# Performance work log

Hardware: AMD Instinct MI355X
Metric: run time of the kernel (lower is better)

The kernel has to match this reference:

```python
import jax, jax.numpy as jnp
import numpy as np

N_NODES = 50000
N_EDGES = 800000
D_NODE = 64
D_EDGE = 64
D_GLOBAL = 16
D_IN = D_EDGE + 2 * D_NODE + D_GLOBAL  # 208
D_HID = 256
D_OUT = 64


def setup_inputs() -> dict:
    key = jax.random.key(0)
    ks = jax.random.split(key, 8)
    x = jax.random.normal(ks[0], (N_NODES, D_NODE), dtype=jnp.float32)
    edge_attr = jax.random.normal(ks[1], (N_EDGES, D_EDGE), dtype=jnp.float32)
    u = jax.random.normal(ks[2], (1, D_GLOBAL), dtype=jnp.float32)
    W1 = jax.random.normal(ks[3], (D_IN, D_HID), dtype=jnp.float32) * (1.0 / np.sqrt(D_IN))
    b1 = jnp.zeros((D_HID,), dtype=jnp.float32)
    W2 = jax.random.normal(ks[4], (D_HID, D_OUT), dtype=jnp.float32) * (1.0 / np.sqrt(D_HID))
    b2 = jnp.zeros((D_OUT,), dtype=jnp.float32)
    edge_index = jax.random.randint(ks[5], (2, N_EDGES), 0, N_NODES, dtype=jnp.int64)
    return {"x": x, "edge_attr": edge_attr, "u": u, "W1": W1, "b1": b1,
            "W2": W2, "b2": b2, "edge_index": edge_index}


def reference(x, edge_attr, u, W1, b1, W2, b2, edge_index):
    E = edge_attr.shape[0]
    recv = x[edge_index[1]]                         # [E, D_NODE] receiver gather
    send = x[edge_index[0]]                         # [E, D_NODE] sender gather
    g = jnp.broadcast_to(u, (E, u.shape[-1]))       # [E, D_GLOBAL] globals broadcast
    collected = jnp.concatenate([edge_attr, recv, send, g], axis=-1)  # [E, 208]
    h = jax.nn.relu(collected @ W1 + b1)            # [E, 256]
    updated_edges = h @ W2 + b2                     # [E, 64]
    return updated_edges
```

## Files before the change

### kernel.cpp

```cpp
#include <hip/hip_runtime.h>
#include <hip/hip_bf16.h>


#define N_EDGES   800000
#define N_TILES   (N_EDGES / 16)
#define K1        192
#define D_HID     256
#define D_OUT     64
#define W1T_LD    200
#define W2T_LD    264
#define WAVES_PB  16
#define BLOCK_T   (WAVES_PB * 64)
#define GRID_MAIN 256

typedef __attribute__((ext_vector_type(8))) short  short8;
typedef __attribute__((ext_vector_type(4))) float  floatx4;

#define WS_W1T_OFF 0
#define WS_W2T_OFF (256 * W1T_LD * 2)
#define WS_B1P_OFF (WS_W2T_OFF + 64 * W2T_LD * 2)

static __device__ __forceinline__ unsigned short f2bf(float f) {
    unsigned u = __builtin_bit_cast(unsigned, f);
    u += 0x7fffu + ((u >> 16) & 1u);
    return (unsigned short)(u >> 16);
}

static __device__ __forceinline__ short8 cvt8(const float* __restrict__ p) {
    const floatx4* p4 = (const floatx4*)p;
    floatx4 f0 = p4[0];
    floatx4 f1 = p4[1];
    union { short8 s8; unsigned short us[8]; } u;
    u.us[0] = f2bf(f0.x); u.us[1] = f2bf(f0.y); u.us[2] = f2bf(f0.z); u.us[3] = f2bf(f0.w);
    u.us[4] = f2bf(f1.x); u.us[5] = f2bf(f1.y); u.us[6] = f2bf(f1.z); u.us[7] = f2bf(f1.w);
    return u.s8;
}

__global__ void edgeblk_prep(const float* __restrict__ W1, const float* __restrict__ b1,
                             const float* __restrict__ W2, const float* __restrict__ u,
                             unsigned short* __restrict__ w1t, unsigned short* __restrict__ w2t,
                             float* __restrict__ b1p) {
    int tid = blockIdx.x * blockDim.x + threadIdx.x;
    int nth = gridDim.x * blockDim.x;
    for (int j = tid; j < 256 * K1; j += nth) {
        int n = j / K1, k = j - n * K1;
        w1t[n * W1T_LD + k] = f2bf(W1[k * 256 + n]);
    }
    for (int j = tid; j < 64 * 256; j += nth) {
        int m = j >> 8, k = j & 255;
        int kap = k & 31, q = kap >> 3, t = kap & 7;
        int rho = (t < 4) ? (q * 4 + t) : (16 + q * 4 + (t - 4));
        int src = (k & ~31) + rho;
        w2t[m * W2T_LD + k] = f2bf(W2[src * 64 + m]);
    }
    for (int n = tid; n < 256; n += nth) {
        float s = b1[n];
        for (int t = 0; t < 16; ++t) s += u[t] * W1[(K1 + t) * 256 + n];
        b1p[n] = s;
    }
}

__global__ __launch_bounds__(BLOCK_T) void edgeblk_mlp(
        const float* __restrict__ x, const float* __restrict__ edge_attr,
        const int* __restrict__ eidx,
        const unsigned short* __restrict__ w1t_g, const unsigned short* __restrict__ w2t_g,
        const float* __restrict__ b1p_g, const float* __restrict__ b2_g,
        float* __restrict__ out) {
    __shared__ alignas(16) unsigned short sW1[256 * W1T_LD];
    __shared__ alignas(16) unsigned short sW2[64 * W2T_LD];
    __shared__ alignas(16) float sB1[256];
    __shared__ alignas(16) float sB2[64];

    {
        const uint4* s1 = (const uint4*)w1t_g;  uint4* d1 = (uint4*)sW1;
        for (int i = threadIdx.x; i < 256 * W1T_LD / 8; i += BLOCK_T) d1[i] = s1[i];
        const uint4* s2 = (const uint4*)w2t_g;  uint4* d2 = (uint4*)sW2;
        for (int i = threadIdx.x; i < 64 * W2T_LD / 8; i += BLOCK_T) d2[i] = s2[i];
        if (threadIdx.x < 256) sB1[threadIdx.x] = b1p_g[threadIdx.x];
        if (threadIdx.x < 64)  sB2[threadIdx.x] = b2_g[threadIdx.x];
    }
    __syncthreads();

    const int wid  = threadIdx.x >> 6;
    const int lane = threadIdx.x & 63;
    const int m    = lane & 15;
    const int quad = lane >> 4;

    float b2v[4];
#pragma unroll
    for (int nt = 0; nt < 4; ++nt) b2v[nt] = sB2[nt * 16 + m];

    const int gw = blockIdx.x * WAVES_PB + wid;
    const int NW = GRID_MAIN * WAVES_PB;

    for (int tile = gw; tile < N_TILES; tile += NW) {
        const int e    = tile * 16 + m;
        const int recv = eidx[N_EDGES + e];
        const int send = eidx[e];
        const float* pe = edge_attr + (long)e    * 64 + quad * 8;
        const float* pr = x         + (long)recv * 64 + quad * 8;
        const float* ps = x         + (long)send * 64 + quad * 8;

        short8 A[6];
        A[0] = cvt8(pe);      A[1] = cvt8(pe + 32);
        A[2] = cvt8(pr);      A[3] = cvt8(pr + 32);
        A[4] = cvt8(ps);      A[5] = cvt8(ps + 32);

        floatx4 oacc[4];
#pragma unroll
        for (int nt = 0; nt < 4; ++nt) oacc[nt] = (floatx4){0.f, 0.f, 0.f, 0.f};

#pragma unroll
        for (int nc = 0; nc < 8; ++nc) {
            floatx4 c0 = (floatx4){0.f, 0.f, 0.f, 0.f};
            floatx4 c1 = (floatx4){0.f, 0.f, 0.f, 0.f};
#pragma unroll
            for (int kt = 0; kt < 6; ++kt) {
                short8 bA = *(const short8*)&sW1[(nc * 32      + m) * W1T_LD + kt * 32 + quad * 8];
                short8 bB = *(const short8*)&sW1[(nc * 32 + 16 + m) * W1T_LD + kt * 32 + quad * 8];
                c0 = __builtin_amdgcn_mfma_f32_16x16x32_bf16(bA, A[kt], c0, 0, 0, 0);
                c1 = __builtin_amdgcn_mfma_f32_16x16x32_bf16(bB, A[kt], c1, 0, 0, 0);
            }
            const floatx4 bias0 = *(const floatx4*)&sB1[nc * 32      + quad * 4];
            const floatx4 bias1 = *(const floatx4*)&sB1[nc * 32 + 16 + quad * 4];
            union { short8 s8; unsigned short us[8]; } a2u;
#pragma unroll
            for (int r = 0; r < 4; ++r) {
                float h0 = c0[r] + bias0[r];
                float h1 = c1[r] + bias1[r];
                h0 = h0 > 0.f ? h0 : 0.f;
                h1 = h1 > 0.f ? h1 : 0.f;
                a2u.us[r]     = f2bf(h0);
                a2u.us[r + 4] = f2bf(h1);
            }
            short8 a2 = a2u.s8;
#pragma unroll
            for (int nt = 0; nt < 4; ++nt) {
                short8 b2f = *(const short8*)&sW2[(nt * 16 + m) * W2T_LD + nc * 32 + quad * 8];
                oacc[nt] = __builtin_amdgcn_mfma_f32_16x16x32_bf16(a2, b2f, oacc[nt], 0, 0, 0);
            }
        }

        float* po = out + (long)tile * 16 * 64;
#pragma unroll
        for (int nt = 0; nt < 4; ++nt) {
#pragma unroll
            for (int r = 0; r < 4; ++r) {
                po[(quad * 4 + r) * 64 + nt * 16 + m] = oacc[nt][r] + b2v[nt];
            }
        }
    }
}

extern "C" void kernel_launch(void* const* d_in, const int* in_sizes, int n_in,
                              void* d_out, int out_size, void* d_ws, size_t ws_size,
                              hipStream_t stream) {
    const float* x   = (const float*)d_in[0];
    const float* ea  = (const float*)d_in[1];
    const float* u   = (const float*)d_in[2];
    const float* W1  = (const float*)d_in[3];
    const float* b1  = (const float*)d_in[4];
    const float* W2  = (const float*)d_in[5];
    const float* b2  = (const float*)d_in[6];
    const int*   ei  = (const int*)d_in[7];
    float* out = (float*)d_out;

    unsigned short* w1t = (unsigned short*)((char*)d_ws + WS_W1T_OFF);
    unsigned short* w2t = (unsigned short*)((char*)d_ws + WS_W2T_OFF);
    float*          b1p = (float*)((char*)d_ws + WS_B1P_OFF);

    hipLaunchKernelGGL(edgeblk_prep, dim3(192), dim3(256), 0, stream,
                       W1, b1, W2, u, w1t, w2t, b1p);
    hipLaunchKernelGGL(edgeblk_mlp, dim3(GRID_MAIN), dim3(BLOCK_T), 0, stream,
                       x, ea, ei, w1t, w2t, b1p, b2, out);
}
```

Before: 2.022 ms.

## Pre-convert node features to bf16, prefetch gathers, transpose output MFMA for vector stores

```diff
diff --git a/kernel.cpp b/kernel.cpp
--- a/kernel.cpp
+++ b/kernel.cpp
@@ -2,6 +2,7 @@
 #include <hip/hip_bf16.h>
 
 
+#define N_NODES   50000
 #define N_EDGES   800000
 #define N_TILES   (N_EDGES / 16)
 #define K1        192
@@ -19,6 +20,7 @@
 #define WS_W1T_OFF 0
 #define WS_W2T_OFF (256 * W1T_LD * 2)
 #define WS_B1P_OFF (WS_W2T_OFF + 64 * W2T_LD * 2)
+#define WS_XB_OFF  (WS_B1P_OFF + 1024)
 
 static __device__ __forceinline__ unsigned short f2bf(float f) {
     unsigned u = __builtin_bit_cast(unsigned, f);
@@ -26,20 +28,25 @@
     return (unsigned short)(u >> 16);
 }
 
-static __device__ __forceinline__ short8 cvt8(const float* __restrict__ p) {
-    const floatx4* p4 = (const floatx4*)p;
-    floatx4 f0 = p4[0];
-    floatx4 f1 = p4[1];
+static __device__ __forceinline__ short8 pack8(floatx4 f0, floatx4 f1) {
     union { short8 s8; unsigned short us[8]; } u;
     u.us[0] = f2bf(f0.x); u.us[1] = f2bf(f0.y); u.us[2] = f2bf(f0.z); u.us[3] = f2bf(f0.w);
     u.us[4] = f2bf(f1.x); u.us[5] = f2bf(f1.y); u.us[6] = f2bf(f1.z); u.us[7] = f2bf(f1.w);
     return u.s8;
 }
 
+static __device__ __forceinline__ short8 cvt8nt(const float* __restrict__ p) {
+    const floatx4* p4 = (const floatx4*)p;
+    floatx4 f0 = __builtin_nontemporal_load(p4);
+    floatx4 f1 = __builtin_nontemporal_load(p4 + 1);
+    return pack8(f0, f1);
+}
+
 __global__ void edgeblk_prep(const float* __restrict__ W1, const float* __restrict__ b1,
                              const float* __restrict__ W2, const float* __restrict__ u,
+                             const float* __restrict__ x,
                              unsigned short* __restrict__ w1t, unsigned short* __restrict__ w2t,
-                             float* __restrict__ b1p) {
+                             float* __restrict__ b1p, unsigned short* __restrict__ xb) {
     int tid = blockIdx.x * blockDim.x + threadIdx.x;
     int nth = gridDim.x * blockDim.x;
     for (int j = tid; j < 256 * K1; j += nth) {
@@ -58,10 +65,15 @@
         for (int t = 0; t < 16; ++t) s += u[t] * W1[(K1 + t) * 256 + n];
         b1p[n] = s;
     }
-}
-
-__global__ __launch_bounds__(BLOCK_T) void edgeblk_mlp(
-        const float* __restrict__ x, const float* __restrict__ edge_attr,
+    short8* xb8 = (short8*)xb;
+    for (int j = tid; j < N_NODES * 64 / 8; j += nth) {
+        const floatx4* p4 = (const floatx4*)(x + j * 8);
+        xb8[j] = pack8(p4[0], p4[1]);
+    }
+}
+
+__global__ __launch_bounds__(BLOCK_T, 4) void edgeblk_mlp(
+        const unsigned short* __restrict__ xb, const float* __restrict__ edge_attr,
         const int* __restrict__ eidx,
         const unsigned short* __restrict__ w1t_g, const unsigned short* __restrict__ w2t_g,
         const float* __restrict__ b1p_g, const float* __restrict__ b2_g,
@@ -86,25 +98,49 @@
     const int m    = lane & 15;
     const int quad = lane >> 4;
 
-    float b2v[4];
-#pragma unroll
-    for (int nt = 0; nt < 4; ++nt) b2v[nt] = sB2[nt * 16 + m];
-
     const int gw = blockIdx.x * WAVES_PB + wid;
     const int NW = GRID_MAIN * WAVES_PB;
 
-    for (int tile = gw; tile < N_TILES; tile += NW) {
-        const int e    = tile * 16 + m;
-        const int recv = eidx[N_EDGES + e];
-        const int send = eidx[e];
-        const float* pe = edge_attr + (long)e    * 64 + quad * 8;
-        const float* pr = x         + (long)recv * 64 + quad * 8;
-        const float* ps = x         + (long)send * 64 + quad * 8;
-
+    int tile = gw;
+    short8 Rp0 = {}, Rp1 = {}, Sp0 = {}, Sp1 = {};
+    int rcv1 = 0, snd1 = 0;
+    if (tile < N_TILES) {
+        int e = tile * 16 + m;
+        int rcv = eidx[N_EDGES + e];
+        int snd = eidx[e];
+        const short8* pr = (const short8*)(xb + (long)rcv * 64 + quad * 8);
+        Rp0 = pr[0]; Rp1 = pr[4];
+        const short8* ps = (const short8*)(xb + (long)snd * 64 + quad * 8);
+        Sp0 = ps[0]; Sp1 = ps[4];
+    }
+    if (tile + NW < N_TILES) {
+        int e = (tile + NW) * 16 + m;
+        rcv1 = eidx[N_EDGES + e];
+        snd1 = eidx[e];
+    }
+
+    for (; tile < N_TILES; tile += NW) {
         short8 A[6];
-        A[0] = cvt8(pe);      A[1] = cvt8(pe + 32);
-        A[2] = cvt8(pr);      A[3] = cvt8(pr + 32);
-        A[4] = cvt8(ps);      A[5] = cvt8(ps + 32);
+        A[2] = Rp0; A[3] = Rp1; A[4] = Sp0; A[5] = Sp1;
+        const float* pe = edge_attr + (long)(tile * 16 + m) * 64 + quad * 8;
+        A[0] = cvt8nt(pe);
+        A[1] = cvt8nt(pe + 32);
+
+        {
+            int tn = tile + NW;
+            if (tn < N_TILES) {
+                const short8* pr = (const short8*)(xb + (long)rcv1 * 64 + quad * 8);
+                Rp0 = pr[0]; Rp1 = pr[4];
+                const short8* ps = (const short8*)(xb + (long)snd1 * 64 + quad * 8);
+                Sp0 = ps[0]; Sp1 = ps[4];
+                int t2 = tn + NW;
+                if (t2 < N_TILES) {
+                    int e2 = t2 * 16 + m;
+                    rcv1 = eidx[N_EDGES + e2];
+                    snd1 = eidx[e2];
+                }
+            }
+        }
 
         floatx4 oacc[4];
 #pragma unroll
@@ -137,17 +173,18 @@
 #pragma unroll
             for (int nt = 0; nt < 4; ++nt) {
                 short8 b2f = *(const short8*)&sW2[(nt * 16 + m) * W2T_LD + nc * 32 + quad * 8];
-                oacc[nt] = __builtin_amdgcn_mfma_f32_16x16x32_bf16(a2, b2f, oacc[nt], 0, 0, 0);
+                oacc[nt] = __builtin_amdgcn_mfma_f32_16x16x32_bf16(b2f, a2, oacc[nt], 0, 0, 0);
             }
         }
 
-        float* po = out + (long)tile * 16 * 64;
+        float* po = out + (long)tile * 16 * 64 + m * 64;
 #pragma unroll
         for (int nt = 0; nt < 4; ++nt) {
-#pragma unroll
-            for (int r = 0; r < 4; ++r) {
-                po[(quad * 4 + r) * 64 + nt * 16 + m] = oacc[nt][r] + b2v[nt];
-            }
+            const floatx4 bb = *(const floatx4*)&sB2[nt * 16 + quad * 4];
+            floatx4 v;
+#pragma unroll
+            for (int r = 0; r < 4; ++r) v[r] = oacc[nt][r] + bb[r];
+            __builtin_nontemporal_store(v, (floatx4*)(po + nt * 16 + quad * 4));
         }
     }
 }
@@ -168,9 +205,10 @@
     unsigned short* w1t = (unsigned short*)((char*)d_ws + WS_W1T_OFF);
     unsigned short* w2t = (unsigned short*)((char*)d_ws + WS_W2T_OFF);
     float*          b1p = (float*)((char*)d_ws + WS_B1P_OFF);
-
-    hipLaunchKernelGGL(edgeblk_prep, dim3(192), dim3(256), 0, stream,
-                       W1, b1, W2, u, w1t, w2t, b1p);
+    unsigned short* xb  = (unsigned short*)((char*)d_ws + WS_XB_OFF);
+
+    hipLaunchKernelGGL(edgeblk_prep, dim3(256), dim3(256), 0, stream,
+                       W1, b1, W2, u, x, w1t, w2t, b1p, xb);
     hipLaunchKernelGGL(edgeblk_mlp, dim3(GRID_MAIN), dim3(BLOCK_T), 0, stream,
-                       x, ea, ei, w1t, w2t, b1p, b2, out);
-}
+                       xb, ea, ei, w1t, w2t, b1p, b2, out);
+}
```

Result: slower. 2.137 ms (+5.7%).

## Pre-convert node features to bf16 and vectorize output stores via swapped MFMA operands

Applied to the files above, without the earlier changes.

```diff
diff --git a/kernel.cpp b/kernel.cpp
--- a/kernel.cpp
+++ b/kernel.cpp
@@ -2,6 +2,7 @@
 #include <hip/hip_bf16.h>
 
 
+#define N_NODES   50000
 #define N_EDGES   800000
 #define N_TILES   (N_EDGES / 16)
 #define K1        192
@@ -19,6 +20,7 @@
 #define WS_W1T_OFF 0
 #define WS_W2T_OFF (256 * W1T_LD * 2)
 #define WS_B1P_OFF (WS_W2T_OFF + 64 * W2T_LD * 2)
+#define WS_XB_OFF  (WS_B1P_OFF + 1024)
 
 static __device__ __forceinline__ unsigned short f2bf(float f) {
     unsigned u = __builtin_bit_cast(unsigned, f);
@@ -26,20 +28,23 @@
     return (unsigned short)(u >> 16);
 }
 
-static __device__ __forceinline__ short8 cvt8(const float* __restrict__ p) {
-    const floatx4* p4 = (const floatx4*)p;
-    floatx4 f0 = p4[0];
-    floatx4 f1 = p4[1];
+static __device__ __forceinline__ short8 pack8(floatx4 f0, floatx4 f1) {
     union { short8 s8; unsigned short us[8]; } u;
     u.us[0] = f2bf(f0.x); u.us[1] = f2bf(f0.y); u.us[2] = f2bf(f0.z); u.us[3] = f2bf(f0.w);
     u.us[4] = f2bf(f1.x); u.us[5] = f2bf(f1.y); u.us[6] = f2bf(f1.z); u.us[7] = f2bf(f1.w);
     return u.s8;
 }
 
+static __device__ __forceinline__ short8 cvt8(const float* __restrict__ p) {
+    const floatx4* p4 = (const floatx4*)p;
+    return pack8(p4[0], p4[1]);
+}
+
 __global__ void edgeblk_prep(const float* __restrict__ W1, const float* __restrict__ b1,
                              const float* __restrict__ W2, const float* __restrict__ u,
+                             const float* __restrict__ x,
                              unsigned short* __restrict__ w1t, unsigned short* __restrict__ w2t,
-                             float* __restrict__ b1p) {
+                             float* __restrict__ b1p, unsigned short* __restrict__ xb) {
     int tid = blockIdx.x * blockDim.x + threadIdx.x;
     int nth = gridDim.x * blockDim.x;
     for (int j = tid; j < 256 * K1; j += nth) {
@@ -58,10 +63,17 @@
         for (int t = 0; t < 16; ++t) s += u[t] * W1[(K1 + t) * 256 + n];
         b1p[n] = s;
     }
+    short8* xb8 = (short8*)xb;
+    for (int j = tid; j < N_NODES * 64 / 8; j += nth) {
+        const floatx4* p4 = (const floatx4*)(x + j * 8);
+        xb8[j] = pack8(p4[0], p4[1]);
+    }
 }
 
-__global__ __launch_bounds__(BLOCK_T) void edgeblk_mlp(
-        const float* __restrict__ x, const float* __restrict__ edge_attr,
+__global__ __launch_bounds__(BLOCK_T)
+__attribute__((amdgpu_waves_per_eu(4, 4)))
+void edgeblk_mlp(
+        const unsigned short* __restrict__ xb, const float* __restrict__ edge_attr,
         const int* __restrict__ eidx,
         const unsigned short* __restrict__ w1t_g, const unsigned short* __restrict__ w2t_g,
         const float* __restrict__ b1p_g, const float* __restrict__ b2_g,
@@ -86,10 +98,6 @@
     const int m    = lane & 15;
     const int quad = lane >> 4;
 
-    float b2v[4];
-#pragma unroll
-    for (int nt = 0; nt < 4; ++nt) b2v[nt] = sB2[nt * 16 + m];
-
     const int gw = blockIdx.x * WAVES_PB + wid;
     const int NW = GRID_MAIN * WAVES_PB;
 
@@ -97,14 +105,17 @@
         const int e    = tile * 16 + m;
         const int recv = eidx[N_EDGES + e];
         const int send = eidx[e];
-        const float* pe = edge_attr + (long)e    * 64 + quad * 8;
-        const float* pr = x         + (long)recv * 64 + quad * 8;
-        const float* ps = x         + (long)send * 64 + quad * 8;
 
         short8 A[6];
-        A[0] = cvt8(pe);      A[1] = cvt8(pe + 32);
-        A[2] = cvt8(pr);      A[3] = cvt8(pr + 32);
-        A[4] = cvt8(ps);      A[5] = cvt8(ps + 32);
+        {
+            const float* pe = edge_attr + (long)e * 64 + quad * 8;
+            A[0] = cvt8(pe);
+            A[1] = cvt8(pe + 32);
+            const short8* pr = (const short8*)(xb + (long)recv * 64 + quad * 8);
+            A[2] = pr[0]; A[3] = pr[4];
+            const short8* ps = (const short8*)(xb + (long)send * 64 + quad * 8);
+            A[4] = ps[0]; A[5] = ps[4];
+        }
 
         floatx4 oacc[4];
 #pragma unroll
@@ -137,17 +148,18 @@
 #pragma unroll
             for (int nt = 0; nt < 4; ++nt) {
                 short8 b2f = *(const short8*)&sW2[(nt * 16 + m) * W2T_LD + nc * 32 + quad * 8];
-                oacc[nt] = __builtin_amdgcn_mfma_f32_16x16x32_bf16(a2, b2f, oacc[nt], 0, 0, 0);
+                oacc[nt] = __builtin_amdgcn_mfma_f32_16x16x32_bf16(b2f, a2, oacc[nt], 0, 0, 0);
             }
         }
 
-        float* po = out + (long)tile * 16 * 64;
+        float* po = out + (long)tile * 16 * 64 + m * 64;
 #pragma unroll
         for (int nt = 0; nt < 4; ++nt) {
+            const floatx4 bb = *(const floatx4*)&sB2[nt * 16 + quad * 4];
+            floatx4 v;
 #pragma unroll
-            for (int r = 0; r < 4; ++r) {
-                po[(quad * 4 + r) * 64 + nt * 16 + m] = oacc[nt][r] + b2v[nt];
-            }
+            for (int r = 0; r < 4; ++r) v[r] = oacc[nt][r] + bb[r];
+            *(floatx4*)(po + nt * 16 + quad * 4) = v;
         }
     }
 }
@@ -168,9 +180,10 @@
     unsigned short* w1t = (unsigned short*)((char*)d_ws + WS_W1T_OFF);
     unsigned short* w2t = (unsigned short*)((char*)d_ws + WS_W2T_OFF);
     float*          b1p = (float*)((char*)d_ws + WS_B1P_OFF);
+    unsigned short* xb  = (unsigned short*)((char*)d_ws + WS_XB_OFF);
 
-    hipLaunchKernelGGL(edgeblk_prep, dim3(192), dim3(256), 0, stream,
-                       W1, b1, W2, u, w1t, w2t, b1p);
+    hipLaunchKernelGGL(edgeblk_prep, dim3(256), dim3(256), 0, stream,
+                       W1, b1, W2, u, x, w1t, w2t, b1p, xb);
     hipLaunchKernelGGL(edgeblk_mlp, dim3(GRID_MAIN), dim3(BLOCK_T), 0, stream,
-                       x, ea, ei, w1t, w2t, b1p, b2, out);
+                       xb, ea, ei, w1t, w2t, b1p, b2, out);
 }
```

After: 2.023 ms. No clear change (+0.1%).
